# Performance work log

Hardware: AMD Instinct MI355X
Metric: run time of the kernel (lower is better)

The kernel has to match this reference:

```python
import jax, jax.numpy as jnp
import numpy as np

D_IN = 1024
D_OUT = 1024
NUM_HEADS = 16
HEAD_DIM = D_OUT // NUM_HEADS
SEQ = 2048
BATCH = 2


def setup_inputs() -> dict:
    key = jax.random.key(0)
    ks = jax.random.split(key, 6)
    s = 1.0 / np.sqrt(D_IN)
    x = jax.random.normal(ks[0], (BATCH, SEQ, D_IN), dtype=jnp.float32)
    Wq = jax.random.uniform(ks[1], (D_IN, D_OUT), jnp.float32, -s, s)
    Wk = jax.random.uniform(ks[2], (D_IN, D_OUT), jnp.float32, -s, s)
    Wv = jax.random.uniform(ks[3], (D_IN, D_OUT), jnp.float32, -s, s)
    Wo = jax.random.uniform(ks[4], (D_OUT, D_OUT), jnp.float32, -s, s)
    bo = jax.random.uniform(ks[5], (D_OUT,), jnp.float32, -s, s)
    return {"x": x, "Wq": Wq, "Wk": Wk, "Wv": Wv, "Wo": Wo, "bo": bo}


def reference(x, Wq, Wk, Wv, Wo, bo):
    b, n, _ = x.shape
    # projections, split into heads: (b, h, n, hd)
    def split_heads(t):
        return t.reshape(b, n, NUM_HEADS, HEAD_DIM).transpose(0, 2, 1, 3)
    q = split_heads(x @ Wq)
    k = split_heads(x @ Wk)
    v = split_heads(x @ Wv)
    scores = jnp.einsum("bhqd,bhkd->bhqk", q, k)
    causal = jnp.triu(jnp.ones((n, n), dtype=bool), k=1)
    scores = jnp.where(causal, -jnp.inf, scores)
    attn = jax.nn.softmax(scores / np.sqrt(HEAD_DIM), axis=-1)
    # dropout prob is 0.0 -> identity
    ctx = jnp.einsum("bhqk,bhkd->bhqd", attn, v)
    ctx = ctx.transpose(0, 2, 1, 3).reshape(b, n, D_OUT)
    return ctx @ Wo + bo
```

## Files before the change

kernel.cpp:

```cpp
#include <hip/hip_runtime.h>
#include <hip/hip_bf16.h>
#include <stdint.h>

#define D_IN   1024
#define D_OUT  1024
#define NHEAD  16
#define HDIM   64
#define SEQ    2048
#define BATCH  2
#define M_TOT  (BATCH*SEQ)

typedef __attribute__((ext_vector_type(8)))  short bfx8;
typedef __attribute__((ext_vector_type(4)))  short bfx4;
typedef __attribute__((ext_vector_type(4)))  float fx4;
typedef __attribute__((ext_vector_type(16))) float fx16;
typedef unsigned short u16;
typedef unsigned int   u32;

__device__ __forceinline__ u16 f2bf(float f) {
    u32 u = __builtin_bit_cast(u32, f);
    u32 r = (u + 0x7FFFu + ((u >> 16) & 1u)) >> 16;
    return (u16)r;
}
__device__ __forceinline__ float bf2f(u16 v) {
    u32 u = (u32)v << 16;
    return __builtin_bit_cast(float, u);
}

__device__ __forceinline__ u32 cvtpk(float lo, float hi) {
    u32 r;
    asm("v_cvt_pk_bf16_f32 %0, %1, %2" : "=v"(r) : "v"(lo), "v"(hi));
    return r;
}

__device__ __forceinline__ float exp2x(float x) {
    float r;
    asm("v_exp_f32 %0, %1" : "=v"(r) : "v"(x));
    return r;
}

__device__ __forceinline__ void gload16(const u16* g, u16* l) {
    __builtin_amdgcn_global_load_lds(
        (const __attribute__((address_space(1))) void*)g,
        (__attribute__((address_space(3))) void*)l, 16, 0, 0);
}

__global__ void k_conv_x(const float* __restrict__ x, u16* __restrict__ xb) {
    int i = blockIdx.x * 256 + threadIdx.x;
    const float4* s = reinterpret_cast<const float4*>(x);
    float4 a = s[2*i], b = s[2*i+1];
    uint4 o;
    o.x = (u32)f2bf(a.x) | ((u32)f2bf(a.y) << 16);
    o.y = (u32)f2bf(a.z) | ((u32)f2bf(a.w) << 16);
    o.z = (u32)f2bf(b.x) | ((u32)f2bf(b.y) << 16);
    o.w = (u32)f2bf(b.z) | ((u32)f2bf(b.w) << 16);
    reinterpret_cast<uint4*>(xb)[i] = o;
}

__global__ void k_conv_wt(const float* __restrict__ Wq, const float* __restrict__ Wk,
                          const float* __restrict__ Wv, const float* __restrict__ Wo,
                          u16* __restrict__ wt) {
    __shared__ float tile[32][33];
    int wsel = blockIdx.z;
    const float* W = (wsel == 0) ? Wq : (wsel == 1) ? Wk : (wsel == 2) ? Wv : Wo;
    const float scale = (wsel == 0) ? 0.125f * 1.4426950408889634f : 1.0f;
    u16* dst = wt + (size_t)wsel * D_IN * D_OUT;
    int r0 = blockIdx.y * 32, c0 = blockIdx.x * 32;
    int tx = threadIdx.x & 31, ty = threadIdx.x >> 5;
    #pragma unroll
    for (int k = 0; k < 4; k++) {
        int i = ty + k * 8;
        tile[i][tx] = W[(size_t)(r0 + i) * D_OUT + c0 + tx];
    }
    __syncthreads();
    #pragma unroll
    for (int k = 0; k < 4; k++) {
        int i = ty + k * 8;
        dst[(size_t)(c0 + i) * D_IN + r0 + tx] = f2bf(tile[tx][i] * scale);
    }
}

__global__ __launch_bounds__(256) void k_qkv(const u16* __restrict__ A,
                                             const u16* __restrict__ Bt,
                                             u16* __restrict__ outb) {
    __shared__ u16 aL[128][32];
    __shared__ u16 bL[128][32];
    const int K = 1024;
    const int nb = blockIdx.x * 128, mb = blockIdx.y * 128;
    const int t = threadIdx.x, lane = t & 63, w = t >> 6;
    const int wr = w >> 1, wc = w & 1;
    const int li = lane & 15, lg = lane >> 4;
    const int srow = lane >> 2, schunk = (lane & 3) * 8;

    fx4 acc[4][4];
    #pragma unroll
    for (int i = 0; i < 4; i++)
        #pragma unroll
        for (int j = 0; j < 4; j++) acc[i][j] = fx4{0.f, 0.f, 0.f, 0.f};

    const u16* aBase = A  + (size_t)(mb + w * 32 + srow) * K + schunk;
    const u16* bBase = Bt + (size_t)(nb + w * 32 + srow) * K + schunk;

    for (int kb = 0; kb < K; kb += 32) {
        #pragma unroll
        for (int c = 0; c < 2; c++) {
            gload16(aBase + (size_t)c * 16 * K + kb, &aL[w * 32 + c * 16][0]);
            gload16(bBase + (size_t)c * 16 * K + kb, &bL[w * 32 + c * 16][0]);
        }
        __syncthreads();
        bfx8 af[4], bf[4];
        #pragma unroll
        for (int mi = 0; mi < 4; mi++)
            af[mi] = *reinterpret_cast<const bfx8*>(&aL[wr * 64 + mi * 16 + li][lg * 8]);
        #pragma unroll
        for (int ni = 0; ni < 4; ni++)
            bf[ni] = *reinterpret_cast<const bfx8*>(&bL[wc * 64 + ni * 16 + li][lg * 8]);
        #pragma unroll
        for (int mi = 0; mi < 4; mi++)
            #pragma unroll
            for (int ni = 0; ni < 4; ni++)
                acc[mi][ni] = __builtin_amdgcn_mfma_f32_16x16x32_bf16(af[mi], bf[ni], acc[mi][ni], 0, 0, 0);
        __syncthreads();
    }

    #pragma unroll
    for (int mi = 0; mi < 4; mi++) {
        #pragma unroll
        for (int ni = 0; ni < 4; ni++) {
            const int n = nb + wc * 64 + ni * 16 + li;
            const int m0 = mb + wr * 64 + mi * 16 + lg * 4;
            const int proj = n >> 10, h = (n >> 6) & 15, d = n & 63;
            const int b = m0 >> 11, s0 = m0 & 2047;
            if (proj == 2) {
                u16* op = outb + (size_t)2 * M_TOT * D_OUT +
                          ((size_t)(b * NHEAD + h) * HDIM + d) * SEQ + s0;
                bfx4 pk = {(short)f2bf(acc[mi][ni][0]), (short)f2bf(acc[mi][ni][1]),
                           (short)f2bf(acc[mi][ni][2]), (short)f2bf(acc[mi][ni][3])};
                *reinterpret_cast<bfx4*>(op) = pk;
            } else {
                u16* op = outb + (size_t)proj * M_TOT * D_OUT;
                #pragma unroll
                for (int r = 0; r < 4; r++)
                    op[((size_t)(b * NHEAD + h) * SEQ + s0 + r) * HDIM + d] =
                        f2bf(acc[mi][ni][r]);
            }
        }
    }
}

__global__ __launch_bounds__(256) void k_oproj(const u16* __restrict__ A,
                                               const u16* __restrict__ Bt,
                                               const float* __restrict__ bias,
                                               float* __restrict__ outf) {
    __shared__ u16 aL[128][32];
    __shared__ u16 bL[64][32];
    const int K = 1024;
    const int nb = blockIdx.x * 64, mb = blockIdx.y * 128;
    const int t = threadIdx.x, lane = t & 63, w = t >> 6;
    const int wr = w >> 1, wc = w & 1;
    const int li = lane & 15, lg = lane >> 4;
    const int srow = lane >> 2, schunk = (lane & 3) * 8;

    fx4 acc[4][2];
    #pragma unroll
    for (int i = 0; i < 4; i++)
        #pragma unroll
        for (int j = 0; j < 2; j++) acc[i][j] = fx4{0.f, 0.f, 0.f, 0.f};

    const u16* aBase = A  + (size_t)(mb + w * 32 + srow) * K + schunk;
    const u16* bBase = Bt + (size_t)(nb + w * 16 + srow) * K + schunk;

    for (int kb = 0; kb < K; kb += 32) {
        gload16(aBase + kb,          &aL[w * 32][0]);
        gload16(aBase + 16 * K + kb, &aL[w * 32 + 16][0]);
        gload16(bBase + kb,          &bL[w * 16][0]);
        __syncthreads();
        bfx8 af[4], bf[2];
        #pragma unroll
        for (int mi = 0; mi < 4; mi++)
            af[mi] = *reinterpret_cast<const bfx8*>(&aL[wr * 64 + mi * 16 + li][lg * 8]);
        #pragma unroll
        for (int ni = 0; ni < 2; ni++)
            bf[ni] = *reinterpret_cast<const bfx8*>(&bL[wc * 32 + ni * 16 + li][lg * 8]);
        #pragma unroll
        for (int mi = 0; mi < 4; mi++)
            #pragma unroll
            for (int ni = 0; ni < 2; ni++)
                acc[mi][ni] = __builtin_amdgcn_mfma_f32_16x16x32_bf16(af[mi], bf[ni], acc[mi][ni], 0, 0, 0);
        __syncthreads();
    }

    #pragma unroll
    for (int mi = 0; mi < 4; mi++) {
        #pragma unroll
        for (int ni = 0; ni < 2; ni++) {
            const int n = nb + wc * 32 + ni * 16 + li;
            const int m0 = mb + wr * 64 + mi * 16 + lg * 4;
            const float bv = bias[n];
            #pragma unroll
            for (int r = 0; r < 4; r++)
                outf[(size_t)(m0 + r) * D_OUT + n] = acc[mi][ni][r] + bv;
        }
    }
}

__global__ __launch_bounds__(512, 2) void k_attn(const u16* __restrict__ Q,
                                                 const u16* __restrict__ Kp,
                                                 const u16* __restrict__ Vt,
                                                 u16* __restrict__ ctx,
                                                 u16* __restrict__ o1,
                                                 float* __restrict__ l0,
                                                 float* __restrict__ l1) {
    __shared__ u16 kbuf[2][64][64];
    __shared__ u16 vbuf[2][64][64];

    static const __constant__ signed char QT[12]   = {7,7,6,6,5,5,4,4,3,2,1,0};
    static const __constant__ signed char PART[12] = {0,1,0,1,0,1,0,1,0,0,0,0};

    const int g  = blockIdx.x;
    const int m  = g & 31, pp = g >> 5;
    const int bh = (m & 7) * 4 + (m >> 3);
    const int qt = QT[pp], part = PART[pp];
    const bool heavy = (qt >= 4);
    const int nt = 4 * qt + 4;
    int t0, t1;
    if (heavy) { int h1 = nt >> 1; t0 = part ? h1 : 0; t1 = part ? nt : h1; }
    else       { t0 = 0; t1 = nt; }
    const int ntL = t1 - t0;

    const size_t base = (size_t)bh * SEQ * HDIM;
    const int t = threadIdx.x, lane = t & 63, w = t >> 6;
    const int l31 = lane & 31, hi = lane >> 5;
    const int srow = lane >> 3;
    const int ts = (lane & 7) ^ srow;
    const int bq = bh >> 4, hh = bh & 15;
    const int swz = (l31 & 7) * 8;
    const int qwb = qt * 256 + w * 32;
    const int qg  = qwb + l31;

    auto stage = [&](int bi, int kvb) {
        const int rb = w * 8;
        gload16(Kp + base + (size_t)(kvb + rb + srow) * HDIM + ts * 8,
                &kbuf[bi][rb][0]);
        gload16(Vt + base + (size_t)(rb + srow) * SEQ + kvb + ts * 8,
                &vbuf[bi][rb][0]);
    };

    bfx8 qf[4];
    #pragma unroll
    for (int dc = 0; dc < 4; dc++)
        qf[dc] = *reinterpret_cast<const bfx8*>(
            &Q[base + (size_t)qg * HDIM + dc * 16 + hi * 8]);
    fx16 cacc[2];
    #pragma unroll
    for (int dt = 0; dt < 2; dt++)
        #pragma unroll
        for (int r = 0; r < 16; r++) cacc[dt][r] = 0.f;
    float lsum = 0.f;

    stage(0, t0 * 64);

    for (int tt = 0; tt < ntL; tt++) {
        const int ti = t0 + tt, kvb = ti * 64;
        if (tt + 1 < ntL) {
            stage((tt + 1) & 1, (ti + 1) * 64);
            asm volatile("s_waitcnt vmcnt(2)" ::: "memory");
        } else {
            asm volatile("s_waitcnt vmcnt(0)" ::: "memory");
        }
        __builtin_amdgcn_s_barrier();
        __builtin_amdgcn_sched_barrier(0);
        const int bi = tt & 1;
        if (kvb <= qwb + 31) {
            fx16 sc[2];
            #pragma unroll
            for (int s = 0; s < 2; s++) {
                #pragma unroll
                for (int r = 0; r < 16; r++) sc[s][r] = 0.f;
                #pragma unroll
                for (int dc = 0; dc < 4; dc++) {
                    bfx8 kf = *reinterpret_cast<const bfx8*>(
                        &kbuf[bi][s * 32 + l31][(dc * 16 + hi * 8) ^ swz]);
                    sc[s] = __builtin_amdgcn_mfma_f32_32x32x16_bf16(kf, qf[dc], sc[s], 0, 0, 0);
                }
            }
            if (kvb + 63 > qwb) {
                #pragma unroll
                for (int s = 0; s < 2; s++)
                    #pragma unroll
                    for (int r = 0; r < 16; r++) {
                        int kvg = kvb + s * 32 + (r & 3) + 8 * (r >> 2) + 4 * hi;
                        if (kvg > qg) sc[s][r] = -1e30f;
                    }
            }
            float ps = 0.f;
            #pragma unroll
            for (int s = 0; s < 2; s++)
                #pragma unroll
                for (int r = 0; r < 16; r++) {
                    float pv = exp2x(sc[s][r]);
                    sc[s][r] = pv;
                    ps += pv;
                }
            lsum += ps;
            #pragma unroll
            for (int c = 0; c < 4; c++) {
                const int s = c >> 1, rb_ = (c & 1) * 8;
                u32 a0 = cvtpk(sc[s][rb_ + 0], sc[s][rb_ + 1]);
                u32 a1 = cvtpk(sc[s][rb_ + 2], sc[s][rb_ + 3]);
                u32 b0 = cvtpk(sc[s][rb_ + 4], sc[s][rb_ + 5]);
                u32 b1 = cvtpk(sc[s][rb_ + 6], sc[s][rb_ + 7]);
                u32 X0 = hi ? a0 : b0, X1 = hi ? a1 : b1;
                u32 Y0 = (u32)__shfl_xor((int)X0, 32);
                u32 Y1 = (u32)__shfl_xor((int)X1, 32);
                uint4 pw;
                pw.x = hi ? Y0 : a0;
                pw.y = hi ? Y1 : a1;
                pw.z = hi ? b0 : Y0;
                pw.w = hi ? b1 : Y1;
                bfx8 pf = __builtin_bit_cast(bfx8, pw);
                #pragma unroll
                for (int dt = 0; dt < 2; dt++) {
                    bfx8 vf = *reinterpret_cast<const bfx8*>(
                        &vbuf[bi][dt * 32 + l31][(c * 16 + hi * 8) ^ swz]);
                    cacc[dt] = __builtin_amdgcn_mfma_f32_32x32x16_bf16(pf, vf, cacc[dt], 0, 0, 0);
                }
            }
        }
        asm volatile("s_waitcnt lgkmcnt(0)" ::: "memory");
        __builtin_amdgcn_s_barrier();
    }

    float ltot = lsum + __shfl_xor(lsum, 32);
    if (!heavy) {
        float linv = 1.0f / ltot;
        #pragma unroll
        for (int r = 0; r < 16; r++) {
            const int qpat = (r & 3) + 8 * (r >> 2) + 4 * hi;
            float rl = __shfl(linv, qpat);
            const int q = qwb + qpat;
            #pragma unroll
            for (int dt = 0; dt < 2; dt++)
                ctx[((size_t)(bq * SEQ + q)) * D_OUT + hh * HDIM + dt * 32 + l31] =
                    f2bf(cacc[dt][r] * rl);
        }
    } else {
        const int qt4 = qt - 4;
        const int rbase = (qt4 * 32 + bh) * 256 + w * 32;
        if (hi == 0) { (part ? l1 : l0)[rbase + l31] = ltot; }
        #pragma unroll
        for (int r = 0; r < 16; r++) {
            const int qpat = (r & 3) + 8 * (r >> 2) + 4 * hi;
            const int q = qwb + qpat;
            #pragma unroll
            for (int dt = 0; dt < 2; dt++) {
                const int d = dt * 32 + l31;
                u16 val = f2bf(cacc[dt][r]);
                if (part == 0)
                    ctx[((size_t)(bq * SEQ + q)) * D_OUT + hh * HDIM + d] = val;
                else
                    o1[((size_t)(rbase + qpat)) * 64 + d] = val;
            }
        }
    }
}

__global__ void k_comb(u16* __restrict__ ctx, const u16* __restrict__ o1,
                       const float* __restrict__ l0, const float* __restrict__ l1) {
    int i = blockIdx.x * 256 + threadIdx.x;
    const int d    = (i & 7) * 8;
    const int qrow = (i >> 3) & 255;
    const int bi_  = i >> 11;
    const int bh   = bi_ & 31, qt4 = bi_ >> 5;
    const int bq = bh >> 4, hh = bh & 15;
    const int token = bq * SEQ + (4 + qt4) * 256 + qrow;
    const size_t cidx = (size_t)token * D_OUT + hh * HDIM + d;
    const int ridx = bi_ * 256 + qrow;
    const size_t oidx = (size_t)ridx * 64 + d;
    const float linv = 1.0f / (l0[ridx] + l1[ridx]);
    bfx8 a = *reinterpret_cast<const bfx8*>(&ctx[cidx]);
    bfx8 b = *reinterpret_cast<const bfx8*>(&o1[oidx]);
    bfx8 o;
    #pragma unroll
    for (int j = 0; j < 8; j++)
        o[j] = (short)f2bf((bf2f((u16)a[j]) + bf2f((u16)b[j])) * linv);
    *reinterpret_cast<bfx8*>(&ctx[cidx]) = o;
}

extern "C" void kernel_launch(void* const* d_in, const int* in_sizes, int n_in,
                              void* d_out, int out_size, void* d_ws, size_t ws_size,
                              hipStream_t stream) {
    const float* x  = (const float*)d_in[0];
    const float* Wq = (const float*)d_in[1];
    const float* Wk = (const float*)d_in[2];
    const float* Wv = (const float*)d_in[3];
    const float* Wo = (const float*)d_in[4];
    const float* bo = (const float*)d_in[5];
    float* out = (float*)d_out;

    char* ws = (char*)d_ws;
    u16* xb   = (u16*)(ws);
    u16* wt   = (u16*)(ws + (8u << 20));
    u16* qkvb = (u16*)(ws + (16u << 20));
    u16* ctxb = (u16*)(ws + (40u << 20));

    u16*   o1p = (u16*)(ws);
    float* l0p = (float*)(ws + (4u << 20));
    float* l1p = (float*)(ws + (4u << 20) + (128u << 10));

    const u16* Qb  = qkvb;
    const u16* Kb  = qkvb + (size_t)M_TOT * D_OUT;
    const u16* Vtb = qkvb + (size_t)2 * M_TOT * D_OUT;

    k_conv_x <<<2048, 256, 0, stream>>>(x, xb);
    k_conv_wt<<<dim3(32, 32, 4), 256, 0, stream>>>(Wq, Wk, Wv, Wo, wt);
    k_qkv    <<<dim3(24, 32), 256, 0, stream>>>(xb, wt, qkvb);
    k_attn   <<<dim3(384), 512, 0, stream>>>(Qb, Kb, Vtb, ctxb, o1p, l0p, l1p);
    k_comb   <<<1024, 256, 0, stream>>>(ctxb, o1p, l0p, l1p);
    k_oproj  <<<dim3(16, 32), 256, 0, stream>>>(
        ctxb, wt + (size_t)3 * D_IN * D_OUT, bo, out);
}
```

Measured before the change: 110.7 us.

## Widen GEMM K-tile with XOR-swizzled LDS and triple-buffer attention KV staging

```diff
diff --git a/kernel.cpp b/kernel.cpp
--- a/kernel.cpp
+++ b/kernel.cpp
@@ -83,14 +83,15 @@
 __global__ __launch_bounds__(256) void k_qkv(const u16* __restrict__ A,
                                              const u16* __restrict__ Bt,
                                              u16* __restrict__ outb) {
-    __shared__ u16 aL[128][32];
-    __shared__ u16 bL[128][32];
+    __shared__ u16 aL[128][64];
+    __shared__ u16 bL[128][64];
     const int K = 1024;
     const int nb = blockIdx.x * 128, mb = blockIdx.y * 128;
     const int t = threadIdx.x, lane = t & 63, w = t >> 6;
     const int wr = w >> 1, wc = w & 1;
     const int li = lane & 15, lg = lane >> 4;
-    const int srow = lane >> 2, schunk = (lane & 3) * 8;
+    const int srow = lane >> 3;
+    const int ts = (lane & 7) ^ srow;
 
     fx4 acc[4][4];
     #pragma unroll
@@ -98,28 +99,41 @@
         #pragma unroll
         for (int j = 0; j < 4; j++) acc[i][j] = fx4{0.f, 0.f, 0.f, 0.f};
 
-    const u16* aBase = A  + (size_t)(mb + w * 32 + srow) * K + schunk;
-    const u16* bBase = Bt + (size_t)(nb + w * 32 + srow) * K + schunk;
-
-    for (int kb = 0; kb < K; kb += 32) {
-        #pragma unroll
-        for (int c = 0; c < 2; c++) {
-            gload16(aBase + (size_t)c * 16 * K + kb, &aL[w * 32 + c * 16][0]);
-            gload16(bBase + (size_t)c * 16 * K + kb, &bL[w * 32 + c * 16][0]);
+    const u16* aBase = A  + (size_t)(mb + w * 32 + srow) * K + ts * 8;
+    const u16* bBase = Bt + (size_t)(nb + w * 32 + srow) * K + ts * 8;
+
+    for (int kb = 0; kb < K; kb += 64) {
+        #pragma unroll
+        for (int i = 0; i < 4; i++) {
+            gload16(aBase + (size_t)i * 8 * K + kb, &aL[w * 32 + i * 8][0]);
+            gload16(bBase + (size_t)i * 8 * K + kb, &bL[w * 32 + i * 8][0]);
         }
         __syncthreads();
-        bfx8 af[4], bf[4];
-        #pragma unroll
-        for (int mi = 0; mi < 4; mi++)
-            af[mi] = *reinterpret_cast<const bfx8*>(&aL[wr * 64 + mi * 16 + li][lg * 8]);
-        #pragma unroll
-        for (int ni = 0; ni < 4; ni++)
-            bf[ni] = *reinterpret_cast<const bfx8*>(&bL[wc * 64 + ni * 16 + li][lg * 8]);
-        #pragma unroll
-        for (int mi = 0; mi < 4; mi++)
-            #pragma unroll
-            for (int ni = 0; ni < 4; ni++)
-                acc[mi][ni] = __builtin_amdgcn_mfma_f32_16x16x32_bf16(af[mi], bf[ni], acc[mi][ni], 0, 0, 0);
+        bfx8 af[4][2], bf[4][2];
+        #pragma unroll
+        for (int mi = 0; mi < 4; mi++) {
+            const int row = wr * 64 + mi * 16 + li;
+            #pragma unroll
+            for (int kh = 0; kh < 2; kh++)
+                af[mi][kh] = *reinterpret_cast<const bfx8*>(
+                    &aL[row][((kh * 4 + lg) ^ (row & 7)) * 8]);
+        }
+        #pragma unroll
+        for (int ni = 0; ni < 4; ni++) {
+            const int row = wc * 64 + ni * 16 + li;
+            #pragma unroll
+            for (int kh = 0; kh < 2; kh++)
+                bf[ni][kh] = *reinterpret_cast<const bfx8*>(
+                    &bL[row][((kh * 4 + lg) ^ (row & 7)) * 8]);
+        }
+        #pragma unroll
+        for (int kh = 0; kh < 2; kh++)
+            #pragma unroll
+            for (int mi = 0; mi < 4; mi++)
+                #pragma unroll
+                for (int ni = 0; ni < 4; ni++)
+                    acc[mi][ni] = __builtin_amdgcn_mfma_f32_16x16x32_bf16(
+                        af[mi][kh], bf[ni][kh], acc[mi][ni], 0, 0, 0);
         __syncthreads();
     }
 
@@ -152,14 +166,15 @@
                                                const u16* __restrict__ Bt,
                                                const float* __restrict__ bias,
                                                float* __restrict__ outf) {
-    __shared__ u16 aL[128][32];
-    __shared__ u16 bL[64][32];
+    __shared__ u16 aL[128][64];
+    __shared__ u16 bL[64][64];
     const int K = 1024;
     const int nb = blockIdx.x * 64, mb = blockIdx.y * 128;
     const int t = threadIdx.x, lane = t & 63, w = t >> 6;
     const int wr = w >> 1, wc = w & 1;
     const int li = lane & 15, lg = lane >> 4;
-    const int srow = lane >> 2, schunk = (lane & 3) * 8;
+    const int srow = lane >> 3;
+    const int ts = (lane & 7) ^ srow;
 
     fx4 acc[4][2];
     #pragma unroll
@@ -167,26 +182,42 @@
         #pragma unroll
         for (int j = 0; j < 2; j++) acc[i][j] = fx4{0.f, 0.f, 0.f, 0.f};
 
-    const u16* aBase = A  + (size_t)(mb + w * 32 + srow) * K + schunk;
-    const u16* bBase = Bt + (size_t)(nb + w * 16 + srow) * K + schunk;
-
-    for (int kb = 0; kb < K; kb += 32) {
-        gload16(aBase + kb,          &aL[w * 32][0]);
-        gload16(aBase + 16 * K + kb, &aL[w * 32 + 16][0]);
-        gload16(bBase + kb,          &bL[w * 16][0]);
+    const u16* aBase = A  + (size_t)(mb + w * 32 + srow) * K + ts * 8;
+    const u16* bBase = Bt + (size_t)(nb + w * 16 + srow) * K + ts * 8;
+
+    for (int kb = 0; kb < K; kb += 64) {
+        #pragma unroll
+        for (int i = 0; i < 4; i++)
+            gload16(aBase + (size_t)i * 8 * K + kb, &aL[w * 32 + i * 8][0]);
+        #pragma unroll
+        for (int i = 0; i < 2; i++)
+            gload16(bBase + (size_t)i * 8 * K + kb, &bL[w * 16 + i * 8][0]);
         __syncthreads();
-        bfx8 af[4], bf[2];
-        #pragma unroll
-        for (int mi = 0; mi < 4; mi++)
-            af[mi] = *reinterpret_cast<const bfx8*>(&aL[wr * 64 + mi * 16 + li][lg * 8]);
-        #pragma unroll
-        for (int ni = 0; ni < 2; ni++)
-            bf[ni] = *reinterpret_cast<const bfx8*>(&bL[wc * 32 + ni * 16 + li][lg * 8]);
-        #pragma unroll
-        for (int mi = 0; mi < 4; mi++)
-            #pragma unroll
-            for (int ni = 0; ni < 2; ni++)
-                acc[mi][ni] = __builtin_amdgcn_mfma_f32_16x16x32_bf16(af[mi], bf[ni], acc[mi][ni], 0, 0, 0);
+        bfx8 af[4][2], bf[2][2];
+        #pragma unroll
+        for (int mi = 0; mi < 4; mi++) {
+            const int row = wr * 64 + mi * 16 + li;
+            #pragma unroll
+            for (int kh = 0; kh < 2; kh++)
+                af[mi][kh] = *reinterpret_cast<const bfx8*>(
+                    &aL[row][((kh * 4 + lg) ^ (row & 7)) * 8]);
+        }
+        #pragma unroll
+        for (int ni = 0; ni < 2; ni++) {
+            const int row = wc * 32 + ni * 16 + li;
+            #pragma unroll
+            for (int kh = 0; kh < 2; kh++)
+                bf[ni][kh] = *reinterpret_cast<const bfx8*>(
+                    &bL[row][((kh * 4 + lg) ^ (row & 7)) * 8]);
+        }
+        #pragma unroll
+        for (int kh = 0; kh < 2; kh++)
+            #pragma unroll
+            for (int mi = 0; mi < 4; mi++)
+                #pragma unroll
+                for (int ni = 0; ni < 2; ni++)
+                    acc[mi][ni] = __builtin_amdgcn_mfma_f32_16x16x32_bf16(
+                        af[mi][kh], bf[ni][kh], acc[mi][ni], 0, 0, 0);
         __syncthreads();
     }
 
@@ -211,8 +242,8 @@
                                                  u16* __restrict__ o1,
                                                  float* __restrict__ l0,
                                                  float* __restrict__ l1) {
-    __shared__ u16 kbuf[2][64][64];
-    __shared__ u16 vbuf[2][64][64];
+    __shared__ u16 kbuf[3][64][64];
+    __shared__ u16 vbuf[3][64][64];
 
     static const __constant__ signed char QT[12]   = {7,7,6,6,5,5,4,4,3,2,1,0};
     static const __constant__ signed char PART[12] = {0,1,0,1,0,1,0,1,0,0,0,0};
@@ -259,20 +290,21 @@
     float lsum = 0.f;
 
     stage(0, t0 * 64);
+    if (ntL > 1) stage(1, (t0 + 1) * 64);
 
     for (int tt = 0; tt < ntL; tt++) {
         const int ti = t0 + tt, kvb = ti * 64;
         if (tt + 1 < ntL) {
-            stage((tt + 1) & 1, (ti + 1) * 64);
             asm volatile("s_waitcnt vmcnt(2)" ::: "memory");
         } else {
             asm volatile("s_waitcnt vmcnt(0)" ::: "memory");
         }
         __builtin_amdgcn_s_barrier();
         __builtin_amdgcn_sched_barrier(0);
-        const int bi = tt & 1;
+        const int bi = tt % 3;
         if (kvb <= qwb + 31) {
             fx16 sc[2];
+            __builtin_amdgcn_s_setprio(1);
             #pragma unroll
             for (int s = 0; s < 2; s++) {
                 #pragma unroll
@@ -284,6 +316,7 @@
                     sc[s] = __builtin_amdgcn_mfma_f32_32x32x16_bf16(kf, qf[dc], sc[s], 0, 0, 0);
                 }
             }
+            __builtin_amdgcn_s_setprio(0);
             if (kvb + 63 > qwb) {
                 #pragma unroll
                 for (int s = 0; s < 2; s++)
@@ -319,16 +352,17 @@
                 pw.z = hi ? b0 : Y0;
                 pw.w = hi ? b1 : Y1;
                 bfx8 pf = __builtin_bit_cast(bfx8, pw);
+                __builtin_amdgcn_s_setprio(1);
                 #pragma unroll
                 for (int dt = 0; dt < 2; dt++) {
                     bfx8 vf = *reinterpret_cast<const bfx8*>(
                         &vbuf[bi][dt * 32 + l31][(c * 16 + hi * 8) ^ swz]);
                     cacc[dt] = __builtin_amdgcn_mfma_f32_32x32x16_bf16(pf, vf, cacc[dt], 0, 0, 0);
                 }
+                __builtin_amdgcn_s_setprio(0);
             }
         }
-        asm volatile("s_waitcnt lgkmcnt(0)" ::: "memory");
-        __builtin_amdgcn_s_barrier();
+        if (tt + 2 < ntL) stage((tt + 2) % 3, (ti + 2) * 64);
     }
 
     float ltot = lsum + __shfl_xor(lsum, 32);
```

After: 113.5 us. 2.5% more time.
